# Kernel optimization log

Measured on AMD Instinct MI355X. Metric: run time of the kernel, lower is better.

Reference implementation:

```python
import jax, jax.numpy as jnp
import numpy as np

MASK_VAL = -2.0**32 + 1.0

def setup_inputs() -> dict:
    key = jax.random.key(0)
    ks = jax.random.split(key, 8)
    B, T, E = 4096, 200, 64
    H1, H2 = 64, 32
    return {
        "query": jax.random.normal(ks[0], (B, 1, E), dtype=jnp.float32),
        "keys": jax.random.normal(ks[1], (B, T, E), dtype=jnp.float32),
        "keys_len": jax.random.randint(ks[2], (B, 1), 0, T, dtype=jnp.int64),
        "W1": jax.random.normal(ks[3], (4 * E, H1), dtype=jnp.float32) * 0.05,
        "b1": jnp.zeros((H1,), dtype=jnp.float32),
        "W2": jax.random.normal(ks[4], (H1, H2), dtype=jnp.float32) * 0.05,
        "b2": jnp.zeros((H2,), dtype=jnp.float32),
        "W3": jax.random.normal(ks[5], (H2, 1), dtype=jnp.float32) * 0.05,
        "b3": jnp.zeros((1,), dtype=jnp.float32),
    }

def reference(query, keys, keys_len, W1, b1, W2, b2, W3, b3):
    B, T, E = keys.shape
    q = jnp.broadcast_to(query, (B, T, E))                      # (B,T,E)
    x = jnp.concatenate([q, keys, q - keys, q * keys], axis=-1)  # (B,T,4E)
    h = jax.nn.relu(jnp.einsum('bti,ih->bth', x, W1) + b1)       # (B,T,H1)
    h = jax.nn.relu(jnp.einsum('bth,ho->bto', h, W2) + b2)       # (B,T,H2)
    score = jnp.einsum('bto,oc->btc', h, W3) + b3                # (B,T,1)
    score = jnp.transpose(score, (0, 2, 1))                      # (B,1,T)
    mask = (jnp.arange(T)[None, :] < keys_len)[:, None, :]       # (B,1,T)
    scores = jnp.where(mask, score, jnp.float32(MASK_VAL))
    scores = jax.nn.softmax(scores, axis=-1)                     # weight_normalization=True
    return jnp.matmul(scores, keys)                              # (B,1,E)
```

## Files before the change

kernel.cpp:

```cpp
#include <hip/hip_runtime.h>

typedef __attribute__((ext_vector_type(8))) short short8_t;
typedef __attribute__((ext_vector_type(4))) float f32x4;

#define MASK_VAL (-4294967295.0f)

__device__ __forceinline__ short f2bf(float x) {
    unsigned u;
    __builtin_memcpy(&u, &x, 4);
    u += 0x7FFFu + ((u >> 16) & 1u);
    return (short)(u >> 16);
}
__device__ __forceinline__ float bf2f(short s) {
    unsigned u = ((unsigned)(unsigned short)s) << 16;
    float f;
    __builtin_memcpy(&f, &u, 4);
    return f;
}

__global__ void prep_fold(const float* __restrict__ W1, const float* __restrict__ W2,
                          void* __restrict__ ws)
{
    short* wkT = (short*)ws;
    short* wdT = wkT + 4096;
    short* w2T = wkT + 8192;
    float* wac = (float*)((char*)ws + 20480);
    const int tid = threadIdx.x;
    for (int idx = tid; idx < 4096; idx += 256) {
        int n = idx & 63, k = idx >> 6;
        float a  = W1[4096  + idx];
        float c  = W1[8192  + idx];
        float d  = W1[12288 + idx];
        wkT[n * 64 + k] = f2bf(a - c);
        wdT[n * 64 + k] = f2bf(d);
        wac[idx] = W1[idx] + c;
    }
    for (int idx = tid; idx < 2048; idx += 256) {
        int o = idx & 31, h = idx >> 5;
        w2T[o * 64 + h] = f2bf(W2[idx]);
    }
}

__global__ __launch_bounds__(256, 3) void attn_main(
    const float* __restrict__ query,
    const float* __restrict__ keys,
    const int*   __restrict__ keys_len,
    const float* __restrict__ b1,
    const float* __restrict__ b2,
    const float* __restrict__ W3,
    const float* __restrict__ b3,
    const void*  __restrict__ ws,
    float* __restrict__ out)
{
    constexpr int STR = 72;
    const short* wkT = (const short*)ws;
    const short* wdT = wkT + 4096;
    const short* w2T = wkT + 8192;
    const float* wac = (const float*)((const char*)ws + 20480);

    __shared__ short Bk[64 * STR];
    __shared__ short Bd[64 * STR];
    __shared__ short W2s[32 * STR];
    __shared__ short h1w[4][16 * STR];
    __shared__ float qs[64], cs[64], b2s[32], w3s[32];
    __shared__ float s_arr[208], wsm[208];
    __shared__ float red[256];
    __shared__ float red4a[4], red4b[4];

    const int b    = blockIdx.x;
    const int tid  = threadIdx.x;
    const int lane = tid & 63;
    const int wid  = tid >> 6;
    const int col  = lane & 15;
    const int quad = lane >> 4;

    if (tid < 16) ((float4*)qs)[tid] = ((const float4*)(query + (size_t)b * 64))[tid];
    for (int c = tid; c < 512; c += 256) {
        int r = c >> 3, ch = (c & 7) * 8;
        *(short8_t*)&Bk[r * STR + ch] = *(const short8_t*)(wkT + r * 64 + ch);
        *(short8_t*)&Bd[r * STR + ch] = *(const short8_t*)(wdT + r * 64 + ch);
    }
    {
        int r = tid >> 3, ch = (tid & 7) * 8;
        *(short8_t*)&W2s[r * STR + ch] = *(const short8_t*)(w2T + r * 64 + ch);
    }
    if (tid < 32) { b2s[tid] = b2[tid]; w3s[tid] = W3[tid]; }
    __syncthreads();

    {
        int g = tid >> 6, h = tid & 63;
        float acc = 0.f;
#pragma unroll
        for (int j = 0; j < 16; ++j) {
            int i = g * 16 + j;
            acc += qs[i] * wac[i * 64 + h];
        }
        red[tid] = acc;
    }
    float4 qv[4];
#pragma unroll
    for (int ks = 0; ks < 2; ++ks) {
        qv[ks * 2]     = *(const float4*)&qs[ks * 32 + quad * 8];
        qv[ks * 2 + 1] = *(const float4*)&qs[ks * 32 + quad * 8 + 4];
    }
    __syncthreads();
    if (tid < 64)
        cs[tid] = b1[tid] + red[tid] + red[64 + tid] + red[128 + tid] + red[192 + tid];
    __syncthreads();

    const float  b3v = b3[0];
    const float* kb  = keys + (size_t)b * 12800;
    short* hw = h1w[wid];
    const int nit = (wid == 0) ? 4 : 3;

    short8_t keep0[4], keep1[4];
    float4 n0, n1, n2, n3;
    {
        int row = wid * 16 + col;
        row = row < 200 ? row : 199;
        const float* kr = kb + row * 64 + quad * 8;
        n0 = *(const float4*)(kr);
        n1 = *(const float4*)(kr + 4);
        n2 = *(const float4*)(kr + 32);
        n3 = *(const float4*)(kr + 36);
    }

#pragma unroll
    for (int j = 0; j < 4; ++j) {
        if (j >= nit) break;
        const int mt = wid + j * 4;
        float4 k0 = n0, k1 = n1, k2 = n2, k3 = n3;
        if (j + 1 < nit) {
            int row = (mt + 4) * 16 + col;
            row = row < 200 ? row : 199;
            const float* kr = kb + row * 64 + quad * 8;
            n0 = *(const float4*)(kr);
            n1 = *(const float4*)(kr + 4);
            n2 = *(const float4*)(kr + 32);
            n3 = *(const float4*)(kr + 36);
        }

        short8_t aK0, aK1, aQ0, aQ1;
        aK0[0] = f2bf(k0.x); aK0[1] = f2bf(k0.y); aK0[2] = f2bf(k0.z); aK0[3] = f2bf(k0.w);
        aK0[4] = f2bf(k1.x); aK0[5] = f2bf(k1.y); aK0[6] = f2bf(k1.z); aK0[7] = f2bf(k1.w);
        aK1[0] = f2bf(k2.x); aK1[1] = f2bf(k2.y); aK1[2] = f2bf(k2.z); aK1[3] = f2bf(k2.w);
        aK1[4] = f2bf(k3.x); aK1[5] = f2bf(k3.y); aK1[6] = f2bf(k3.z); aK1[7] = f2bf(k3.w);
        aQ0[0] = f2bf(k0.x * qv[0].x); aQ0[1] = f2bf(k0.y * qv[0].y);
        aQ0[2] = f2bf(k0.z * qv[0].z); aQ0[3] = f2bf(k0.w * qv[0].w);
        aQ0[4] = f2bf(k1.x * qv[1].x); aQ0[5] = f2bf(k1.y * qv[1].y);
        aQ0[6] = f2bf(k1.z * qv[1].z); aQ0[7] = f2bf(k1.w * qv[1].w);
        aQ1[0] = f2bf(k2.x * qv[2].x); aQ1[1] = f2bf(k2.y * qv[2].y);
        aQ1[2] = f2bf(k2.z * qv[2].z); aQ1[3] = f2bf(k2.w * qv[2].w);
        aQ1[4] = f2bf(k3.x * qv[3].x); aQ1[5] = f2bf(k3.y * qv[3].y);
        aQ1[6] = f2bf(k3.z * qv[3].z); aQ1[7] = f2bf(k3.w * qv[3].w);
        keep0[j] = aK0;
        keep1[j] = aK1;

        f32x4 acc[4] = {f32x4{0,0,0,0}, f32x4{0,0,0,0}, f32x4{0,0,0,0}, f32x4{0,0,0,0}};
#pragma unroll
        for (int nt = 0; nt < 4; ++nt) {
            const short* bp = &Bk[(nt * 16 + col) * STR + quad * 8];
            const short* dp = &Bd[(nt * 16 + col) * STR + quad * 8];
            acc[nt] = __builtin_amdgcn_mfma_f32_16x16x32_bf16(aK0, *(const short8_t*)bp,        acc[nt], 0, 0, 0);
            acc[nt] = __builtin_amdgcn_mfma_f32_16x16x32_bf16(aK1, *(const short8_t*)(bp + 32), acc[nt], 0, 0, 0);
            acc[nt] = __builtin_amdgcn_mfma_f32_16x16x32_bf16(aQ0, *(const short8_t*)dp,        acc[nt], 0, 0, 0);
            acc[nt] = __builtin_amdgcn_mfma_f32_16x16x32_bf16(aQ1, *(const short8_t*)(dp + 32), acc[nt], 0, 0, 0);
        }

#pragma unroll
        for (int nt = 0; nt < 4; ++nt) {
            float cadd = cs[nt * 16 + col];
#pragma unroll
            for (int r = 0; r < 4; ++r)
                hw[(quad * 4 + r) * STR + nt * 16 + col] = f2bf(fmaxf(acc[nt][r] + cadd, 0.f));
        }

        f32x4 acc2[2] = {f32x4{0,0,0,0}, f32x4{0,0,0,0}};
#pragma unroll
        for (int ks = 0; ks < 2; ++ks) {
            short8_t a2 = *(const short8_t*)&hw[col * STR + ks * 32 + quad * 8];
            acc2[0] = __builtin_amdgcn_mfma_f32_16x16x32_bf16(
                a2, *(const short8_t*)&W2s[col * STR + ks * 32 + quad * 8], acc2[0], 0, 0, 0);
            acc2[1] = __builtin_amdgcn_mfma_f32_16x16x32_bf16(
                a2, *(const short8_t*)&W2s[(16 + col) * STR + ks * 32 + quad * 8], acc2[1], 0, 0, 0);
        }
#pragma unroll
        for (int r = 0; r < 4; ++r) {
            float v = fmaxf(acc2[0][r] + b2s[col], 0.f) * w3s[col]
                    + fmaxf(acc2[1][r] + b2s[16 + col], 0.f) * w3s[16 + col];
            v += __shfl_xor(v, 1);
            v += __shfl_xor(v, 2);
            v += __shfl_xor(v, 4);
            v += __shfl_xor(v, 8);
            if (col == 0) s_arr[mt * 16 + quad * 4 + r] = v + b3v;
        }
    }
    __syncthreads();

    int len = keys_len[b];
    float val = (tid < 200) ? ((tid < len) ? s_arr[tid] : MASK_VAL) : -INFINITY;
    float m = val;
    for (int off = 32; off >= 1; off >>= 1) m = fmaxf(m, __shfl_xor(m, off));
    if (lane == 0) red4a[wid] = m;
    __syncthreads();
    m = fmaxf(fmaxf(red4a[0], red4a[1]), fmaxf(red4a[2], red4a[3]));
    float p = (tid < 200) ? __expf(val - m) : 0.0f;
    float ssum = p;
    for (int off = 32; off >= 1; off >>= 1) ssum += __shfl_xor(ssum, off);
    if (lane == 0) red4b[wid] = ssum;
    __syncthreads();
    float S = red4b[0] + red4b[1] + red4b[2] + red4b[3];
    if (tid < 200) wsm[tid] = p / S;
    __syncthreads();

    {
        float accv[16];
#pragma unroll
        for (int i = 0; i < 16; ++i) accv[i] = 0.f;
#pragma unroll
        for (int j = 0; j < 4; ++j) {
            if (j >= nit) break;
            int row = (wid + j * 4) * 16 + col;
            float w = (row < 200) ? wsm[row] : 0.f;
            short8_t f0 = keep0[j], f1 = keep1[j];
#pragma unroll
            for (int i = 0; i < 8; ++i) {
                accv[i]     += w * bf2f(f0[i]);
                accv[8 + i] += w * bf2f(f1[i]);
            }
        }
#pragma unroll
        for (int i = 0; i < 16; ++i) {
            float v = accv[i];
            v += __shfl_xor(v, 1);
            v += __shfl_xor(v, 2);
            v += __shfl_xor(v, 4);
            v += __shfl_xor(v, 8);
            accv[i] = v;
        }
        if (col == 0) {
#pragma unroll
            for (int i = 0; i < 8; ++i) {
                red[wid * 64 + quad * 8 + i]      = accv[i];
                red[wid * 64 + 32 + quad * 8 + i] = accv[8 + i];
            }
        }
        __syncthreads();
        if (tid < 64)
            out[(size_t)b * 64 + tid] = red[tid] + red[64 + tid] + red[128 + tid] + red[192 + tid];
    }
}

extern "C" void kernel_launch(void* const* d_in, const int* in_sizes, int n_in,
                              void* d_out, int out_size, void* d_ws, size_t ws_size,
                              hipStream_t stream) {
    const float* query    = (const float*)d_in[0];
    const float* keys     = (const float*)d_in[1];
    const int*   keys_len = (const int*)d_in[2];
    const float* W1       = (const float*)d_in[3];
    const float* b1       = (const float*)d_in[4];
    const float* W2       = (const float*)d_in[5];
    const float* b2       = (const float*)d_in[6];
    const float* W3       = (const float*)d_in[7];
    const float* b3       = (const float*)d_in[8];
    float* out            = (float*)d_out;

    const int B = in_sizes[1] / 12800;

    prep_fold<<<dim3(1), dim3(256), 0, stream>>>(W1, W2, d_ws);
    attn_main<<<dim3(B), dim3(256), 0, stream>>>(
        query, keys, keys_len, b1, b2, W3, b3, d_ws, out);
}
```

Baseline: 330.6 us.

## Assign one wavefront per batch row with online softmax over key tiles

Each block now processes four batch rows, one per wavefront. Each wave loops over all 13 key tiles and keeps a running max, sum and weighted accumulation of keys (online softmax), so the block-wide reductions, the shared score arrays and most __syncthreads are gone. W2 fragments and the bias/W3 values are held in registers instead of shared memory, and launch bounds move to 4 waves per SIMD. The trade is a longer serial loop per wave, plus extra rescale and shuffle work on every tile.

```diff
diff --git a/kernel.cpp b/kernel.cpp
--- a/kernel.cpp
+++ b/kernel.cpp
@@ -4,6 +4,7 @@
 typedef __attribute__((ext_vector_type(4))) float f32x4;
 
 #define MASK_VAL (-4294967295.0f)
+#define NEG_BIG  (-1e30f)
 
 __device__ __forceinline__ short f2bf(float x) {
     unsigned u;
@@ -41,7 +42,7 @@
     }
 }
 
-__global__ __launch_bounds__(256, 3) void attn_main(
+__global__ __launch_bounds__(256, 4) void attn_main(
     const float* __restrict__ query,
     const float* __restrict__ keys,
     const int*   __restrict__ keys_len,
@@ -50,7 +51,8 @@
     const float* __restrict__ W3,
     const float* __restrict__ b3,
     const void*  __restrict__ ws,
-    float* __restrict__ out)
+    float* __restrict__ out,
+    int B)
 {
     constexpr int STR = 72;
     const short* wkT = (const short*)ws;
@@ -60,78 +62,74 @@
 
     __shared__ short Bk[64 * STR];
     __shared__ short Bd[64 * STR];
-    __shared__ short W2s[32 * STR];
     __shared__ short h1w[4][16 * STR];
-    __shared__ float qs[64], cs[64], b2s[32], w3s[32];
-    __shared__ float s_arr[208], wsm[208];
-    __shared__ float red[256];
-    __shared__ float red4a[4], red4b[4];
-
-    const int b    = blockIdx.x;
+    __shared__ float qs[4][64];
+    __shared__ float csw[4][64];
+    __shared__ float swv[4][16];
+
     const int tid  = threadIdx.x;
     const int lane = tid & 63;
     const int wid  = tid >> 6;
     const int col  = lane & 15;
     const int quad = lane >> 4;
-
-    if (tid < 16) ((float4*)qs)[tid] = ((const float4*)(query + (size_t)b * 64))[tid];
+    const int b    = blockIdx.x * 4 + wid;
+    const bool act = (b < B);
+
     for (int c = tid; c < 512; c += 256) {
         int r = c >> 3, ch = (c & 7) * 8;
         *(short8_t*)&Bk[r * STR + ch] = *(const short8_t*)(wkT + r * 64 + ch);
         *(short8_t*)&Bd[r * STR + ch] = *(const short8_t*)(wdT + r * 64 + ch);
     }
-    {
-        int r = tid >> 3, ch = (tid & 7) * 8;
-        *(short8_t*)&W2s[r * STR + ch] = *(const short8_t*)(w2T + r * 64 + ch);
-    }
-    if (tid < 32) { b2s[tid] = b2[tid]; w3s[tid] = W3[tid]; }
+
+    const float* kb = nullptr;
+    float4 n0, n1, n2, n3;
+    float b2a = 0.f, b2b = 0.f, w3a = 0.f, w3b = 0.f, b3v = 0.f;
+    short8_t w2f00, w2f01, w2f10, w2f11;
+    if (act) {
+        kb = keys + (size_t)b * 12800;
+        if (lane < 16)
+            ((float4*)&qs[wid][0])[lane] = ((const float4*)(query + (size_t)b * 64))[lane];
+        {
+            const float* kr = kb + col * 64 + quad * 8;
+            n0 = *(const float4*)(kr);
+            n1 = *(const float4*)(kr + 4);
+            n2 = *(const float4*)(kr + 32);
+            n3 = *(const float4*)(kr + 36);
+        }
+        b2a = b2[col];      b2b = b2[col + 16];
+        w3a = W3[col];      w3b = W3[col + 16];
+        b3v = b3[0];
+        w2f00 = *(const short8_t*)(w2T + col * 64 + quad * 8);
+        w2f01 = *(const short8_t*)(w2T + (16 + col) * 64 + quad * 8);
+        w2f10 = *(const short8_t*)(w2T + col * 64 + 32 + quad * 8);
+        w2f11 = *(const short8_t*)(w2T + (16 + col) * 64 + 32 + quad * 8);
+
+        float acc = b1[lane];
+#pragma unroll 16
+        for (int i = 0; i < 64; ++i)
+            acc += qs[wid][i] * wac[i * 64 + lane];
+        csw[wid][lane] = acc;
+    }
     __syncthreads();
-
-    {
-        int g = tid >> 6, h = tid & 63;
-        float acc = 0.f;
-#pragma unroll
-        for (int j = 0; j < 16; ++j) {
-            int i = g * 16 + j;
-            acc += qs[i] * wac[i * 64 + h];
-        }
-        red[tid] = acc;
-    }
-    float4 qv[4];
-#pragma unroll
-    for (int ks = 0; ks < 2; ++ks) {
-        qv[ks * 2]     = *(const float4*)&qs[ks * 32 + quad * 8];
-        qv[ks * 2 + 1] = *(const float4*)&qs[ks * 32 + quad * 8 + 4];
-    }
-    __syncthreads();
-    if (tid < 64)
-        cs[tid] = b1[tid] + red[tid] + red[64 + tid] + red[128 + tid] + red[192 + tid];
-    __syncthreads();
-
-    const float  b3v = b3[0];
-    const float* kb  = keys + (size_t)b * 12800;
+    if (!act) return;
+
+    const float4 qv0 = *(const float4*)&qs[wid][quad * 8];
+    const float4 qv1 = *(const float4*)&qs[wid][quad * 8 + 4];
+    const float4 qv2 = *(const float4*)&qs[wid][32 + quad * 8];
+    const float4 qv3 = *(const float4*)&qs[wid][32 + quad * 8 + 4];
+
+    const int len = keys_len[b];
     short* hw = h1w[wid];
-    const int nit = (wid == 0) ? 4 : 3;
-
-    short8_t keep0[4], keep1[4];
-    float4 n0, n1, n2, n3;
-    {
-        int row = wid * 16 + col;
-        row = row < 200 ? row : 199;
-        const float* kr = kb + row * 64 + quad * 8;
-        n0 = *(const float4*)(kr);
-        n1 = *(const float4*)(kr + 4);
-        n2 = *(const float4*)(kr + 32);
-        n3 = *(const float4*)(kr + 36);
-    }
-
-#pragma unroll
-    for (int j = 0; j < 4; ++j) {
-        if (j >= nit) break;
-        const int mt = wid + j * 4;
+
+    float m_run = NEG_BIG, l_run = 0.f;
+    float accv[16];
+#pragma unroll
+    for (int i = 0; i < 16; ++i) accv[i] = 0.f;
+
+    for (int jt = 0; jt < 13; ++jt) {
         float4 k0 = n0, k1 = n1, k2 = n2, k3 = n3;
-        if (j + 1 < nit) {
-            int row = (mt + 4) * 16 + col;
+        if (jt < 12) {
+            int row = jt * 16 + 16 + col;
             row = row < 200 ? row : 199;
             const float* kr = kb + row * 64 + quad * 8;
             n0 = *(const float4*)(kr);
@@ -145,16 +143,14 @@
         aK0[4] = f2bf(k1.x); aK0[5] = f2bf(k1.y); aK0[6] = f2bf(k1.z); aK0[7] = f2bf(k1.w);
         aK1[0] = f2bf(k2.x); aK1[1] = f2bf(k2.y); aK1[2] = f2bf(k2.z); aK1[3] = f2bf(k2.w);
         aK1[4] = f2bf(k3.x); aK1[5] = f2bf(k3.y); aK1[6] = f2bf(k3.z); aK1[7] = f2bf(k3.w);
-        aQ0[0] = f2bf(k0.x * qv[0].x); aQ0[1] = f2bf(k0.y * qv[0].y);
-        aQ0[2] = f2bf(k0.z * qv[0].z); aQ0[3] = f2bf(k0.w * qv[0].w);
-        aQ0[4] = f2bf(k1.x * qv[1].x); aQ0[5] = f2bf(k1.y * qv[1].y);
-        aQ0[6] = f2bf(k1.z * qv[1].z); aQ0[7] = f2bf(k1.w * qv[1].w);
-        aQ1[0] = f2bf(k2.x * qv[2].x); aQ1[1] = f2bf(k2.y * qv[2].y);
-        aQ1[2] = f2bf(k2.z * qv[2].z); aQ1[3] = f2bf(k2.w * qv[2].w);
-        aQ1[4] = f2bf(k3.x * qv[3].x); aQ1[5] = f2bf(k3.y * qv[3].y);
-        aQ1[6] = f2bf(k3.z * qv[3].z); aQ1[7] = f2bf(k3.w * qv[3].w);
-        keep0[j] = aK0;
-        keep1[j] = aK1;
+        aQ0[0] = f2bf(k0.x * qv0.x); aQ0[1] = f2bf(k0.y * qv0.y);
+        aQ0[2] = f2bf(k0.z * qv0.z); aQ0[3] = f2bf(k0.w * qv0.w);
+        aQ0[4] = f2bf(k1.x * qv1.x); aQ0[5] = f2bf(k1.y * qv1.y);
+        aQ0[6] = f2bf(k1.z * qv1.z); aQ0[7] = f2bf(k1.w * qv1.w);
+        aQ1[0] = f2bf(k2.x * qv2.x); aQ1[1] = f2bf(k2.y * qv2.y);
+        aQ1[2] = f2bf(k2.z * qv2.z); aQ1[3] = f2bf(k2.w * qv2.w);
+        aQ1[4] = f2bf(k3.x * qv3.x); aQ1[5] = f2bf(k3.y * qv3.y);
+        aQ1[6] = f2bf(k3.z * qv3.z); aQ1[7] = f2bf(k3.w * qv3.w);
 
         f32x4 acc[4] = {f32x4{0,0,0,0}, f32x4{0,0,0,0}, f32x4{0,0,0,0}, f32x4{0,0,0,0}};
 #pragma unroll
@@ -169,85 +165,80 @@
 
 #pragma unroll
         for (int nt = 0; nt < 4; ++nt) {
-            float cadd = cs[nt * 16 + col];
+            float cadd = csw[wid][nt * 16 + col];
 #pragma unroll
             for (int r = 0; r < 4; ++r)
                 hw[(quad * 4 + r) * STR + nt * 16 + col] = f2bf(fmaxf(acc[nt][r] + cadd, 0.f));
         }
 
-        f32x4 acc2[2] = {f32x4{0,0,0,0}, f32x4{0,0,0,0}};
-#pragma unroll
-        for (int ks = 0; ks < 2; ++ks) {
-            short8_t a2 = *(const short8_t*)&hw[col * STR + ks * 32 + quad * 8];
-            acc2[0] = __builtin_amdgcn_mfma_f32_16x16x32_bf16(
-                a2, *(const short8_t*)&W2s[col * STR + ks * 32 + quad * 8], acc2[0], 0, 0, 0);
-            acc2[1] = __builtin_amdgcn_mfma_f32_16x16x32_bf16(
-                a2, *(const short8_t*)&W2s[(16 + col) * STR + ks * 32 + quad * 8], acc2[1], 0, 0, 0);
-        }
+        f32x4 acc2a = f32x4{0,0,0,0}, acc2b = f32x4{0,0,0,0};
+        {
+            short8_t a20 = *(const short8_t*)&hw[col * STR + quad * 8];
+            acc2a = __builtin_amdgcn_mfma_f32_16x16x32_bf16(a20, w2f00, acc2a, 0, 0, 0);
+            acc2b = __builtin_amdgcn_mfma_f32_16x16x32_bf16(a20, w2f01, acc2b, 0, 0, 0);
+            short8_t a21 = *(const short8_t*)&hw[col * STR + 32 + quad * 8];
+            acc2a = __builtin_amdgcn_mfma_f32_16x16x32_bf16(a21, w2f10, acc2a, 0, 0, 0);
+            acc2b = __builtin_amdgcn_mfma_f32_16x16x32_bf16(a21, w2f11, acc2b, 0, 0, 0);
+        }
+
 #pragma unroll
         for (int r = 0; r < 4; ++r) {
-            float v = fmaxf(acc2[0][r] + b2s[col], 0.f) * w3s[col]
-                    + fmaxf(acc2[1][r] + b2s[16 + col], 0.f) * w3s[16 + col];
+            float v = fmaxf(acc2a[r] + b2a, 0.f) * w3a
+                    + fmaxf(acc2b[r] + b2b, 0.f) * w3b;
             v += __shfl_xor(v, 1);
             v += __shfl_xor(v, 2);
             v += __shfl_xor(v, 4);
             v += __shfl_xor(v, 8);
-            if (col == 0) s_arr[mt * 16 + quad * 4 + r] = v + b3v;
-        }
-    }
-    __syncthreads();
-
-    int len = keys_len[b];
-    float val = (tid < 200) ? ((tid < len) ? s_arr[tid] : MASK_VAL) : -INFINITY;
-    float m = val;
-    for (int off = 32; off >= 1; off >>= 1) m = fmaxf(m, __shfl_xor(m, off));
-    if (lane == 0) red4a[wid] = m;
-    __syncthreads();
-    m = fmaxf(fmaxf(red4a[0], red4a[1]), fmaxf(red4a[2], red4a[3]));
-    float p = (tid < 200) ? __expf(val - m) : 0.0f;
-    float ssum = p;
-    for (int off = 32; off >= 1; off >>= 1) ssum += __shfl_xor(ssum, off);
-    if (lane == 0) red4b[wid] = ssum;
-    __syncthreads();
-    float S = red4b[0] + red4b[1] + red4b[2] + red4b[3];
-    if (tid < 200) wsm[tid] = p / S;
-    __syncthreads();
-
-    {
-        float accv[16];
-#pragma unroll
-        for (int i = 0; i < 16; ++i) accv[i] = 0.f;
-#pragma unroll
-        for (int j = 0; j < 4; ++j) {
-            if (j >= nit) break;
-            int row = (wid + j * 4) * 16 + col;
-            float w = (row < 200) ? wsm[row] : 0.f;
-            short8_t f0 = keep0[j], f1 = keep1[j];
-#pragma unroll
-            for (int i = 0; i < 8; ++i) {
-                accv[i]     += w * bf2f(f0[i]);
-                accv[8 + i] += w * bf2f(f1[i]);
-            }
-        }
-#pragma unroll
-        for (int i = 0; i < 16; ++i) {
-            float v = accv[i];
-            v += __shfl_xor(v, 1);
-            v += __shfl_xor(v, 2);
-            v += __shfl_xor(v, 4);
-            v += __shfl_xor(v, 8);
-            accv[i] = v;
-        }
-        if (col == 0) {
-#pragma unroll
-            for (int i = 0; i < 8; ++i) {
-                red[wid * 64 + quad * 8 + i]      = accv[i];
-                red[wid * 64 + 32 + quad * 8 + i] = accv[8 + i];
-            }
-        }
-        __syncthreads();
-        if (tid < 64)
-            out[(size_t)b * 64 + tid] = red[tid] + red[64 + tid] + red[128 + tid] + red[192 + tid];
+            if (col == 0) swv[wid][quad * 4 + r] = v + b3v;
+        }
+        float sv = swv[wid][col];
+
+        int  row  = jt * 16 + col;
+        bool vrow = row < 200;
+        sv = (row < len) ? sv : MASK_VAL;
+        float svm = vrow ? sv : NEG_BIG;
+        svm = fmaxf(svm, __shfl_xor(svm, 1));
+        svm = fmaxf(svm, __shfl_xor(svm, 2));
+        svm = fmaxf(svm, __shfl_xor(svm, 4));
+        svm = fmaxf(svm, __shfl_xor(svm, 8));
+        float m_new = fmaxf(m_run, svm);
+        float p = vrow ? __expf(sv - m_new) : 0.f;
+        float ps = p;
+        ps += __shfl_xor(ps, 1);
+        ps += __shfl_xor(ps, 2);
+        ps += __shfl_xor(ps, 4);
+        ps += __shfl_xor(ps, 8);
+        if (m_new > m_run) {
+            float scale = __expf(m_run - m_new);
+            l_run *= scale;
+#pragma unroll
+            for (int i = 0; i < 16; ++i) accv[i] *= scale;
+            m_run = m_new;
+        }
+        l_run += ps;
+#pragma unroll
+        for (int i = 0; i < 8; ++i) {
+            accv[i]     += p * bf2f(aK0[i]);
+            accv[8 + i] += p * bf2f(aK1[i]);
+        }
+    }
+
+    float inv = 1.f / l_run;
+#pragma unroll
+    for (int i = 0; i < 16; ++i) {
+        float v = accv[i];
+        v += __shfl_xor(v, 1);
+        v += __shfl_xor(v, 2);
+        v += __shfl_xor(v, 4);
+        v += __shfl_xor(v, 8);
+        accv[i] = v * inv;
+    }
+    if (col == 0) {
+        float* op = out + (size_t)b * 64;
+        *(float4*)(op + quad * 8)          = make_float4(accv[0],  accv[1],  accv[2],  accv[3]);
+        *(float4*)(op + quad * 8 + 4)      = make_float4(accv[4],  accv[5],  accv[6],  accv[7]);
+        *(float4*)(op + 32 + quad * 8)     = make_float4(accv[8],  accv[9],  accv[10], accv[11]);
+        *(float4*)(op + 32 + quad * 8 + 4) = make_float4(accv[12], accv[13], accv[14], accv[15]);
     }
 }
 
@@ -268,6 +259,6 @@
     const int B = in_sizes[1] / 12800;
 
     prep_fold<<<dim3(1), dim3(256), 0, stream>>>(W1, W2, d_ws);
-    attn_main<<<dim3(B), dim3(256), 0, stream>>>(
-        query, keys, keys_len, b1, b2, W3, b3, d_ws, out);
-}
+    attn_main<<<dim3((B + 3) / 4), dim3(256), 0, stream>>>(
+        query, keys, keys_len, b1, b2, W3, b3, d_ws, out, B);
+}
```

New measurement: 448.0 us. +35.5%, slower.
